# Optimization experiments

Hardware: AMD Instinct MI355X
Metric: run time of the kernel (lower is better)

## Reference

```python
import jax, jax.numpy as jnp
import numpy as np

B, S, E, H = 4, 2048, 1024, 16
DK = E // H

def setup_inputs() -> dict:
    key = jax.random.key(0)
    ks = jax.random.split(key, 5)
    scale = 1.0 / np.sqrt(E)
    return {
        "x":  jax.random.normal(ks[0], (B, S, E), dtype=jnp.float32),
        "Wq": jax.random.normal(ks[1], (E, E), dtype=jnp.float32) * scale,
        "Wk": jax.random.normal(ks[2], (E, E), dtype=jnp.float32) * scale,
        "Wv": jax.random.normal(ks[3], (E, E), dtype=jnp.float32) * scale,
        "Wo": jax.random.normal(ks[4], (E, E), dtype=jnp.float32) * scale,
    }

def reference(x, Wq, Wk, Wv, Wo):
    b, s, e = x.shape
    # nn.Linear (no bias): y = x @ W.T
    def split_heads(t):  # (b, s, e) -> (b, H, s, DK)
        return t.reshape(b, s, H, DK).transpose(0, 2, 1, 3)
    Q = split_heads(x @ Wq.T)
    K = split_heads(x @ Wk.T)
    V = split_heads(x @ Wv.T)
    scores = jnp.einsum('bhqd,bhkd->bhqk', Q, K) / jnp.sqrt(jnp.float32(DK))
    attn = jax.nn.softmax(scores, axis=-1)  # dropout p=0.0 -> identity
    ctx = jnp.einsum('bhqk,bhkd->bhqd', attn, V)
    concat = ctx.transpose(0, 2, 1, 3).reshape(b, s, e)
    return concat @ Wo.T
```

## Files before the change

### kernel.cpp

```cpp
#include <hip/hip_runtime.h>


typedef __bf16 bf16x8 __attribute__((ext_vector_type(8)));
typedef __bf16 bf16x4 __attribute__((ext_vector_type(4)));
typedef float floatx4 __attribute__((ext_vector_type(4)));

#define GLOAD_LDS16(gp, lp) __builtin_amdgcn_global_load_lds( \
    (const __attribute__((address_space(1))) unsigned int*)(gp), \
    (__attribute__((address_space(3))) unsigned int*)(lp), 16, 0, 0)

__global__ __launch_bounds__(256) void cvt_x(const float4* __restrict__ s,
                                             bf16x4* __restrict__ d, int n4) {
    int i = blockIdx.x * 256 + threadIdx.x;
    if (i < n4) {
        float4 v = s[i];
        bf16x4 o = { (__bf16)v.x, (__bf16)v.y, (__bf16)v.z, (__bf16)v.w };
        d[i] = o;
    }
}

__global__ __launch_bounds__(256) void cvt_w(const float4* __restrict__ Wq,
                                             const float4* __restrict__ Wk,
                                             const float4* __restrict__ Wv,
                                             const float4* __restrict__ Wo,
                                             bf16x4* __restrict__ oq, bf16x4* __restrict__ ok,
                                             bf16x4* __restrict__ ov, bf16x4* __restrict__ oo,
                                             float qscale) {
    int y = blockIdx.y;
    const float4* s = (y == 0) ? Wq : (y == 1) ? Wk : (y == 2) ? Wv : Wo;
    bf16x4* d = (y == 0) ? oq : (y == 1) ? ok : (y == 2) ? ov : oo;
    float scale = (y == 0) ? qscale : 1.0f;
    int i = blockIdx.x * 256 + threadIdx.x;
    float4 v = s[i];
    bf16x4 o = { (__bf16)(v.x * scale), (__bf16)(v.y * scale),
                 (__bf16)(v.z * scale), (__bf16)(v.w * scale) };
    d[i] = o;
}


__device__ __forceinline__ void gemm_mainloop(const __bf16* __restrict__ A,
                                              const __bf16* __restrict__ W,
                                              __bf16* Asm, __bf16* Bsm,
                                              int bm, int bn, int tid,
                                              floatx4 acc[4][4]) {
    const int w = tid >> 6, lane = tid & 63;
    const int quad = lane >> 4, l15 = lane & 15;
    const int wy = w >> 1, wx = w & 1;
#pragma unroll
    for (int i = 0; i < 4; ++i)
#pragma unroll
        for (int j = 0; j < 4; ++j) acc[i][j] = (floatx4){0.f, 0.f, 0.f, 0.f};

    for (int k0 = 0; k0 < 1024; k0 += 32) {
        __syncthreads();
#pragma unroll
        for (int j = 0; j < 2; ++j) {
            int base = j * 256 + w * 64;
            int flat = base + lane;
            int c = flat >> 7, r = flat & 127;
            GLOAD_LDS16(A + (size_t)(bm + r) * 1024 + k0 + c * 8, (char*)Asm + base * 16);
            GLOAD_LDS16(W + (size_t)(bn + r) * 1024 + k0 + c * 8, (char*)Bsm + base * 16);
        }
        __syncthreads();

        bf16x8 af[4], bf[4];
#pragma unroll
        for (int mt = 0; mt < 4; ++mt)
            af[mt] = *(const bf16x8*)(Asm + (quad * 128 + wy * 64 + mt * 16 + l15) * 8);
#pragma unroll
        for (int nt = 0; nt < 4; ++nt)
            bf[nt] = *(const bf16x8*)(Bsm + (quad * 128 + wx * 64 + nt * 16 + l15) * 8);
#pragma unroll
        for (int mt = 0; mt < 4; ++mt)
#pragma unroll
            for (int nt = 0; nt < 4; ++nt)
                acc[mt][nt] = __builtin_amdgcn_mfma_f32_16x16x32_bf16(af[mt], bf[nt],
                                                                      acc[mt][nt], 0, 0, 0);
    }
    __syncthreads();
}

__global__ __launch_bounds__(256) void gemm_qkv(const __bf16* __restrict__ A,
                                                const __bf16* __restrict__ Wqb,
                                                const __bf16* __restrict__ Wkb,
                                                const __bf16* __restrict__ Wvb,
                                                __bf16* __restrict__ Qg,
                                                __bf16* __restrict__ Kg,
                                                __bf16* __restrict__ Vtg) {
    __shared__ alignas(16) __bf16 Asm[4096];
    __shared__ alignas(16) __bf16 Bsm[4096];
    const int sel = blockIdx.y >> 3;
    const __bf16* W = (sel == 0) ? Wqb : (sel == 1) ? Wkb : Wvb;
    __bf16* ob = (sel == 0) ? Qg : (sel == 1) ? Kg : Vtg;
    const int bm = blockIdx.x * 128, bn = (blockIdx.y & 7) * 128;
    const int tid = threadIdx.x;
    const int w = tid >> 6, lane = tid & 63;
    const int quad = lane >> 4, l15 = lane & 15;
    const int wy = w >> 1, wx = w & 1;

    floatx4 acc[4][4];
    gemm_mainloop(A, W, Asm, Bsm, bm, bn, tid, acc);

    float* tb = (float*)Asm + w * 272;
    const int rr = lane >> 2, c0 = (lane & 3) * 4;
#pragma unroll
    for (int mt = 0; mt < 4; ++mt)
#pragma unroll
        for (int nt = 0; nt < 4; ++nt) {
            if (sel == 2) {
#pragma unroll
                for (int r = 0; r < 4; ++r) tb[l15 * 17 + quad * 4 + r] = acc[mt][nt][r];
            } else {
#pragma unroll
                for (int r = 0; r < 4; ++r) tb[(quad * 4 + r) * 17 + l15] = acc[mt][nt][r];
            }
            float f0 = tb[rr * 17 + c0 + 0], f1 = tb[rr * 17 + c0 + 1];
            float f2 = tb[rr * 17 + c0 + 2], f3 = tb[rr * 17 + c0 + 3];
            bf16x4 pk = { (__bf16)f0, (__bf16)f1, (__bf16)f2, (__bf16)f3 };
            if (sel <= 1) {
                int m = bm + wy * 64 + mt * 16 + rr;
                int n0 = bn + wx * 64 + nt * 16 + c0;
                int bI = m >> 11, s = m & 2047, h = n0 >> 6, d0 = n0 & 63;
                *(bf16x4*)(ob + ((size_t)(bI * 16 + h) * 2048 + s) * 64 + d0) = pk;
            } else {
                int m0 = bm + wy * 64 + mt * 16 + c0;
                int n = bn + wx * 64 + nt * 16 + rr;
                int bI = m0 >> 11, s0 = m0 & 2047, h = n >> 6, d = n & 63;
                *(bf16x4*)(ob + ((size_t)(bI * 16 + h) * 64 + d) * 2048 + s0) = pk;
            }
        }
}

template <int MODE>
__global__ __launch_bounds__(256) void gemm_bt(const __bf16* __restrict__ A,
                                               const __bf16* __restrict__ W,
                                               void* __restrict__ outp) {
    __shared__ alignas(16) __bf16 Asm[4096];
    __shared__ alignas(16) __bf16 Bsm[4096];
    const int tid = threadIdx.x;
    const int lane = tid & 63, w = tid >> 6;
    const int quad = lane >> 4, l15 = lane & 15;
    const int wy = w >> 1, wx = w & 1;
    const int bm = blockIdx.x * 128, bn = blockIdx.y * 128;

    floatx4 acc[4][4];
    gemm_mainloop(A, W, Asm, Bsm, bm, bn, tid, acc);

    float* of = (float*)outp;
#pragma unroll
    for (int mt = 0; mt < 4; ++mt)
#pragma unroll
        for (int nt = 0; nt < 4; ++nt)
#pragma unroll
            for (int r = 0; r < 4; ++r) {
                int m = bm + wy * 64 + mt * 16 + quad * 4 + r;
                int n = bn + wx * 64 + nt * 16 + l15;
                of[(size_t)m * 1024 + n] = acc[mt][nt][r];
            }
}


__device__ __forceinline__ int paddr(int c, int row) {
    int r2 = row ^ (((row >> 3) & 1) << 1) ^ (c & 1);
    return (c * 32 + r2) * 16;
}

__global__ __launch_bounds__(256, 4) void attn_kernel(const __bf16* __restrict__ Qg,
                                                      const __bf16* __restrict__ Kg,
                                                      const __bf16* __restrict__ Vtg,
                                                      __bf16* __restrict__ ctxg) {
    __shared__ alignas(16) __bf16 Ksm[4096];
    __shared__ alignas(16) __bf16 Vsm[4096];
    __shared__ alignas(16) __bf16 Pex[4096];
    const int tid = threadIdx.x;
    const int w = tid >> 6, lane = tid & 63;
    const int quad = lane >> 4, l15 = lane & 15;
    const int qbase = blockIdx.x * 128;
    const int bh = blockIdx.y;

    char* Pw = (w < 2) ? ((char*)Ksm + w * 4096) : ((char*)Pex + (w - 2) * 4096);

    bf16x8 qf[2][2];
#pragma unroll
    for (int mt = 0; mt < 2; ++mt) {
        const __bf16* qrow = Qg + ((size_t)bh * 2048 + qbase + w * 32 + mt * 16 + l15) * 64;
        qf[mt][0] = *(const bf16x8*)(qrow + quad * 8);
        qf[mt][1] = *(const bf16x8*)(qrow + 32 + quad * 8);
    }

    float l_p[2][4] = {{0.f, 0.f, 0.f, 0.f}, {0.f, 0.f, 0.f, 0.f}};
    floatx4 o[2][4];
#pragma unroll
    for (int mt = 0; mt < 2; ++mt)
#pragma unroll
        for (int dt = 0; dt < 4; ++dt) o[mt][dt] = (floatx4){0.f, 0.f, 0.f, 0.f};

    for (int kv = 0; kv < 32; ++kv) {
        const int kv0 = kv * 64;
        __syncthreads();
#pragma unroll
        for (int j = 0; j < 2; ++j) {
            int base = j * 256 + w * 64;
            int flat = base + lane;
            int c = flat >> 6, r = flat & 63;
            GLOAD_LDS16(Kg + ((size_t)bh * 2048 + kv0 + r) * 64 + c * 8, (char*)Ksm + base * 16);
            GLOAD_LDS16(Vtg + ((size_t)bh * 64 + r) * 2048 + kv0 + c * 8, (char*)Vsm + base * 16);
        }
        __syncthreads();

        floatx4 sa[2][4];
#pragma unroll
        for (int mt = 0; mt < 2; ++mt)
#pragma unroll
            for (int nt = 0; nt < 4; ++nt) sa[mt][nt] = (floatx4){0.f, 0.f, 0.f, 0.f};
#pragma unroll
        for (int nt = 0; nt < 4; ++nt) {
            bf16x8 kb0 = *(const bf16x8*)(Ksm + (quad * 64 + nt * 16 + l15) * 8);
            bf16x8 kb1 = *(const bf16x8*)(Ksm + ((4 + quad) * 64 + nt * 16 + l15) * 8);
#pragma unroll
            for (int mt = 0; mt < 2; ++mt) {
                sa[mt][nt] = __builtin_amdgcn_mfma_f32_16x16x32_bf16(qf[mt][0], kb0,
                                                                    sa[mt][nt], 0, 0, 0);
                sa[mt][nt] = __builtin_amdgcn_mfma_f32_16x16x32_bf16(qf[mt][1], kb1,
                                                                    sa[mt][nt], 0, 0, 0);
            }
        }

        __syncthreads();

#pragma unroll
        for (int mt = 0; mt < 2; ++mt)
#pragma unroll
            for (int nt = 0; nt < 4; ++nt)
#pragma unroll
                for (int r = 0; r < 4; ++r) {
                    float p = __builtin_amdgcn_exp2f(sa[mt][nt][r]);
                    l_p[mt][r] += p;
                    unsigned u = __builtin_bit_cast(unsigned, p);
                    *(unsigned short*)(Pw + paddr(nt * 2 + (l15 >> 3),
                                                  mt * 16 + quad * 4 + r)
                                       + (l15 & 7) * 2) = (unsigned short)(u >> 16);
                }

#pragma unroll
        for (int kk = 0; kk < 2; ++kk) {
            bf16x8 pa0 = *(const bf16x8*)(Pw + paddr(kk * 4 + quad, l15));
            bf16x8 pa1 = *(const bf16x8*)(Pw + paddr(kk * 4 + quad, 16 + l15));
#pragma unroll
            for (int dt = 0; dt < 4; ++dt) {
                bf16x8 vb = *(const bf16x8*)(Vsm + ((kk * 4 + quad) * 64 + dt * 16 + l15) * 8);
                o[0][dt] = __builtin_amdgcn_mfma_f32_16x16x32_bf16(pa0, vb, o[0][dt], 0, 0, 0);
                o[1][dt] = __builtin_amdgcn_mfma_f32_16x16x32_bf16(pa1, vb, o[1][dt], 0, 0, 0);
            }
        }
    }

    __syncthreads();

    float inv[2][4];
#pragma unroll
    for (int mt = 0; mt < 2; ++mt)
#pragma unroll
        for (int r = 0; r < 4; ++r) {
            float t = l_p[mt][r];
            t += __shfl_xor(t, 1); t += __shfl_xor(t, 2);
            t += __shfl_xor(t, 4); t += __shfl_xor(t, 8);
            inv[mt][r] = 1.f / t;
        }

    float* tb = (float*)Ksm + w * 272;
    const int bI = bh >> 4, h = bh & 15;
    const int rr = lane >> 2, c0 = (lane & 3) * 4;
#pragma unroll
    for (int mt = 0; mt < 2; ++mt)
#pragma unroll
        for (int dt = 0; dt < 4; ++dt) {
#pragma unroll
            for (int r = 0; r < 4; ++r)
                tb[(quad * 4 + r) * 17 + l15] = o[mt][dt][r] * inv[mt][r];
            float f0 = tb[rr * 17 + c0 + 0], f1 = tb[rr * 17 + c0 + 1];
            float f2 = tb[rr * 17 + c0 + 2], f3 = tb[rr * 17 + c0 + 3];
            bf16x4 pk = { (__bf16)f0, (__bf16)f1, (__bf16)f2, (__bf16)f3 };
            *(bf16x4*)(ctxg + ((size_t)(bI * 2048 + qbase + w * 32 + mt * 16 + rr)) * 1024
                       + h * 64 + dt * 16 + c0) = pk;
        }
}

extern "C" void kernel_launch(void* const* d_in, const int* in_sizes, int n_in,
                              void* d_out, int out_size, void* d_ws, size_t ws_size,
                              hipStream_t stream) {
    const float* x  = (const float*)d_in[0];
    const float* Wq = (const float*)d_in[1];
    const float* Wk = (const float*)d_in[2];
    const float* Wv = (const float*)d_in[3];
    const float* Wo = (const float*)d_in[4];
    float* out = (float*)d_out;
    char* ws = (char*)d_ws;

    __bf16* xb  = (__bf16*)(ws);
    __bf16* wqb = (__bf16*)(ws + (16u << 20));
    __bf16* wkb = (__bf16*)(ws + (18u << 20));
    __bf16* wvb = (__bf16*)(ws + (20u << 20));
    __bf16* wob = (__bf16*)(ws + (22u << 20));
    __bf16* Qg  = (__bf16*)(ws + (24u << 20));
    __bf16* Kg  = (__bf16*)(ws + (40u << 20));
    __bf16* Vtg = (__bf16*)(ws + (56u << 20));
    __bf16* ctx = xb;

    const float qscale = 0.18033688011112042f;

    cvt_x<<<8192, 256, 0, stream>>>((const float4*)x, (bf16x4*)xb, 2097152);
    cvt_w<<<dim3(1024, 4), 256, 0, stream>>>((const float4*)Wq, (const float4*)Wk,
                                             (const float4*)Wv, (const float4*)Wo,
                                             (bf16x4*)wqb, (bf16x4*)wkb,
                                             (bf16x4*)wvb, (bf16x4*)wob, qscale);

    gemm_qkv<<<dim3(64, 24), 256, 0, stream>>>(xb, wqb, wkb, wvb, Qg, Kg, Vtg);

    attn_kernel<<<dim3(16, 64), 256, 0, stream>>>(Qg, Kg, Vtg, ctx);

    gemm_bt<3><<<dim3(64, 8), 256, 0, stream>>>(ctx, wob, (void*)out);
}
```

Measured before the change: 337.6 us.

## Double-buffer GEMM LDS tiles and give attention its own P buffer

The shared GEMM mainloop now keeps two LDS stages and issues the global-to-LDS loads for tile k+1 before computing on tile k, with one barrier per iteration instead of two. The aim is to overlap global memory latency with MFMA work in the QKV and output projections, and the launch bounds now ask for 5 blocks per SM. The attention kernel gets a dedicated P scratch buffer instead of reusing the K tile for two waves, which lets it drop one __syncthreads per KV step. The cost is twice the LDS per GEMM block and more LDS in attention, which may lower occupancy.

```diff
diff --git a/kernel.cpp b/kernel.cpp
--- a/kernel.cpp
+++ b/kernel.cpp
@@ -38,9 +38,26 @@
 }
 
 
+__device__ __forceinline__ void gemm_stage(const __bf16* __restrict__ A,
+                                           const __bf16* __restrict__ W,
+                                           __bf16* SM, int buf,
+                                           int bm, int bn, int k0,
+                                           int w, int lane) {
+#pragma unroll
+    for (int j = 0; j < 2; ++j) {
+        int base = j * 256 + w * 64;
+        int flat = base + lane;
+        int c = flat >> 7, r = flat & 127;
+        GLOAD_LDS16(A + (size_t)(bm + r) * 1024 + k0 + c * 8,
+                    (char*)(SM + buf * 8192) + base * 16);
+        GLOAD_LDS16(W + (size_t)(bn + r) * 1024 + k0 + c * 8,
+                    (char*)(SM + buf * 8192 + 4096) + base * 16);
+    }
+}
+
 __device__ __forceinline__ void gemm_mainloop(const __bf16* __restrict__ A,
                                               const __bf16* __restrict__ W,
-                                              __bf16* Asm, __bf16* Bsm,
+                                              __bf16* SM,
                                               int bm, int bn, int tid,
                                               floatx4 acc[4][4]) {
     const int w = tid >> 6, lane = tid & 63;
@@ -51,18 +68,14 @@
 #pragma unroll
         for (int j = 0; j < 4; ++j) acc[i][j] = (floatx4){0.f, 0.f, 0.f, 0.f};
 
-    for (int k0 = 0; k0 < 1024; k0 += 32) {
-        __syncthreads();
-#pragma unroll
-        for (int j = 0; j < 2; ++j) {
-            int base = j * 256 + w * 64;
-            int flat = base + lane;
-            int c = flat >> 7, r = flat & 127;
-            GLOAD_LDS16(A + (size_t)(bm + r) * 1024 + k0 + c * 8, (char*)Asm + base * 16);
-            GLOAD_LDS16(W + (size_t)(bn + r) * 1024 + k0 + c * 8, (char*)Bsm + base * 16);
-        }
-        __syncthreads();
-
+    gemm_stage(A, W, SM, 0, bm, bn, 0, w, lane);
+    __syncthreads();
+
+    for (int k = 0; k < 32; ++k) {
+        if (k + 1 < 32) gemm_stage(A, W, SM, (k + 1) & 1, bm, bn, (k + 1) * 32, w, lane);
+
+        const __bf16* Asm = SM + (k & 1) * 8192;
+        const __bf16* Bsm = Asm + 4096;
         bf16x8 af[4], bf[4];
 #pragma unroll
         for (int mt = 0; mt < 4; ++mt)
@@ -76,19 +89,18 @@
             for (int nt = 0; nt < 4; ++nt)
                 acc[mt][nt] = __builtin_amdgcn_mfma_f32_16x16x32_bf16(af[mt], bf[nt],
                                                                       acc[mt][nt], 0, 0, 0);
-    }
-    __syncthreads();
-}
-
-__global__ __launch_bounds__(256) void gemm_qkv(const __bf16* __restrict__ A,
-                                                const __bf16* __restrict__ Wqb,
-                                                const __bf16* __restrict__ Wkb,
-                                                const __bf16* __restrict__ Wvb,
-                                                __bf16* __restrict__ Qg,
-                                                __bf16* __restrict__ Kg,
-                                                __bf16* __restrict__ Vtg) {
-    __shared__ alignas(16) __bf16 Asm[4096];
-    __shared__ alignas(16) __bf16 Bsm[4096];
+        __syncthreads();
+    }
+}
+
+__global__ __launch_bounds__(256, 5) void gemm_qkv(const __bf16* __restrict__ A,
+                                                   const __bf16* __restrict__ Wqb,
+                                                   const __bf16* __restrict__ Wkb,
+                                                   const __bf16* __restrict__ Wvb,
+                                                   __bf16* __restrict__ Qg,
+                                                   __bf16* __restrict__ Kg,
+                                                   __bf16* __restrict__ Vtg) {
+    __shared__ alignas(16) __bf16 SM[16384];
     const int sel = blockIdx.y >> 3;
     const __bf16* W = (sel == 0) ? Wqb : (sel == 1) ? Wkb : Wvb;
     __bf16* ob = (sel == 0) ? Qg : (sel == 1) ? Kg : Vtg;
@@ -99,9 +111,9 @@
     const int wy = w >> 1, wx = w & 1;
 
     floatx4 acc[4][4];
-    gemm_mainloop(A, W, Asm, Bsm, bm, bn, tid, acc);
-
-    float* tb = (float*)Asm + w * 272;
+    gemm_mainloop(A, W, SM, bm, bn, tid, acc);
+
+    float* tb = (float*)SM + w * 272;
     const int rr = lane >> 2, c0 = (lane & 3) * 4;
 #pragma unroll
     for (int mt = 0; mt < 4; ++mt)
@@ -132,11 +144,10 @@
 }
 
 template <int MODE>
-__global__ __launch_bounds__(256) void gemm_bt(const __bf16* __restrict__ A,
-                                               const __bf16* __restrict__ W,
-                                               void* __restrict__ outp) {
-    __shared__ alignas(16) __bf16 Asm[4096];
-    __shared__ alignas(16) __bf16 Bsm[4096];
+__global__ __launch_bounds__(256, 5) void gemm_bt(const __bf16* __restrict__ A,
+                                                  const __bf16* __restrict__ W,
+                                                  void* __restrict__ outp) {
+    __shared__ alignas(16) __bf16 SM[16384];
     const int tid = threadIdx.x;
     const int lane = tid & 63, w = tid >> 6;
     const int quad = lane >> 4, l15 = lane & 15;
@@ -144,7 +155,7 @@
     const int bm = blockIdx.x * 128, bn = blockIdx.y * 128;
 
     floatx4 acc[4][4];
-    gemm_mainloop(A, W, Asm, Bsm, bm, bn, tid, acc);
+    gemm_mainloop(A, W, SM, bm, bn, tid, acc);
 
     float* of = (float*)outp;
 #pragma unroll
@@ -171,14 +182,14 @@
                                                       __bf16* __restrict__ ctxg) {
     __shared__ alignas(16) __bf16 Ksm[4096];
     __shared__ alignas(16) __bf16 Vsm[4096];
-    __shared__ alignas(16) __bf16 Pex[4096];
+    __shared__ alignas(16) __bf16 Psm[8192];
     const int tid = threadIdx.x;
     const int w = tid >> 6, lane = tid & 63;
     const int quad = lane >> 4, l15 = lane & 15;
     const int qbase = blockIdx.x * 128;
     const int bh = blockIdx.y;
 
-    char* Pw = (w < 2) ? ((char*)Ksm + w * 4096) : ((char*)Pex + (w - 2) * 4096);
+    char* Pw = (char*)Psm + w * 4096;
 
     bf16x8 qf[2][2];
 #pragma unroll
@@ -225,8 +236,6 @@
                                                                     sa[mt][nt], 0, 0, 0);
             }
         }
-
-        __syncthreads();
 
 #pragma unroll
         for (int mt = 0; mt < 2; ++mt)
```

Result: slower. 347.0 us (+2.8%).

## Widen GEMM tiles to 128x256 and give attention a dedicated P buffer

Applied to the files above, without the earlier changes.

Both projection GEMMs now use 128x256 block tiles: each wave computes 64x128 with 4x8 MFMA accumulators, and the grid is reordered so N-blocks vary fastest. This is meant to raise arithmetic intensity per LDS load and improve reuse of the A rows. The attention kernel gets its own 16KB P scratch buffer instead of aliasing the K shared memory, which removes one __syncthreads per KV iteration. The cost is more shared memory and registers per block (launch bounds of 2 for the GEMMs), so occupancy drops. Fewer GEMM blocks also risks filling the CUs less evenly.

```diff
diff --git a/kernel.cpp b/kernel.cpp
--- a/kernel.cpp
+++ b/kernel.cpp
@@ -38,18 +38,20 @@
 }
 
 
-__device__ __forceinline__ void gemm_mainloop(const __bf16* __restrict__ A,
-                                              const __bf16* __restrict__ W,
-                                              __bf16* Asm, __bf16* Bsm,
-                                              int bm, int bn, int tid,
-                                              floatx4 acc[4][4]) {
+__device__ __forceinline__ void gemm_mainloop2(const __bf16* __restrict__ A,
+                                               const __bf16* __restrict__ W,
+                                               __bf16* SM,
+                                               int bm, int bn, int tid,
+                                               floatx4 acc[4][8]) {
     const int w = tid >> 6, lane = tid & 63;
     const int quad = lane >> 4, l15 = lane & 15;
     const int wy = w >> 1, wx = w & 1;
+    __bf16* Asm = SM;
+    __bf16* Bsm = SM + 4096;
 #pragma unroll
     for (int i = 0; i < 4; ++i)
 #pragma unroll
-        for (int j = 0; j < 4; ++j) acc[i][j] = (floatx4){0.f, 0.f, 0.f, 0.f};
+        for (int j = 0; j < 8; ++j) acc[i][j] = (floatx4){0.f, 0.f, 0.f, 0.f};
 
     for (int k0 = 0; k0 < 1024; k0 += 32) {
         __syncthreads();
@@ -59,54 +61,59 @@
             int flat = base + lane;
             int c = flat >> 7, r = flat & 127;
             GLOAD_LDS16(A + (size_t)(bm + r) * 1024 + k0 + c * 8, (char*)Asm + base * 16);
+        }
+#pragma unroll
+        for (int j = 0; j < 4; ++j) {
+            int base = j * 256 + w * 64;
+            int flat = base + lane;
+            int c = flat >> 8, r = flat & 255;
             GLOAD_LDS16(W + (size_t)(bn + r) * 1024 + k0 + c * 8, (char*)Bsm + base * 16);
         }
         __syncthreads();
 
-        bf16x8 af[4], bf[4];
+        bf16x8 af[4], bf[8];
 #pragma unroll
         for (int mt = 0; mt < 4; ++mt)
             af[mt] = *(const bf16x8*)(Asm + (quad * 128 + wy * 64 + mt * 16 + l15) * 8);
 #pragma unroll
-        for (int nt = 0; nt < 4; ++nt)
-            bf[nt] = *(const bf16x8*)(Bsm + (quad * 128 + wx * 64 + nt * 16 + l15) * 8);
+        for (int nt = 0; nt < 8; ++nt)
+            bf[nt] = *(const bf16x8*)(Bsm + (quad * 256 + wx * 128 + nt * 16 + l15) * 8);
 #pragma unroll
         for (int mt = 0; mt < 4; ++mt)
 #pragma unroll
-            for (int nt = 0; nt < 4; ++nt)
+            for (int nt = 0; nt < 8; ++nt)
                 acc[mt][nt] = __builtin_amdgcn_mfma_f32_16x16x32_bf16(af[mt], bf[nt],
                                                                       acc[mt][nt], 0, 0, 0);
     }
     __syncthreads();
 }
 
-__global__ __launch_bounds__(256) void gemm_qkv(const __bf16* __restrict__ A,
-                                                const __bf16* __restrict__ Wqb,
-                                                const __bf16* __restrict__ Wkb,
-                                                const __bf16* __restrict__ Wvb,
-                                                __bf16* __restrict__ Qg,
-                                                __bf16* __restrict__ Kg,
-                                                __bf16* __restrict__ Vtg) {
-    __shared__ alignas(16) __bf16 Asm[4096];
-    __shared__ alignas(16) __bf16 Bsm[4096];
-    const int sel = blockIdx.y >> 3;
+__global__ __launch_bounds__(256, 2) void gemm_qkv(const __bf16* __restrict__ A,
+                                                   const __bf16* __restrict__ Wqb,
+                                                   const __bf16* __restrict__ Wkb,
+                                                   const __bf16* __restrict__ Wvb,
+                                                   __bf16* __restrict__ Qg,
+                                                   __bf16* __restrict__ Kg,
+                                                   __bf16* __restrict__ Vtg) {
+    __shared__ alignas(16) __bf16 SM[12288];
+    const int sel = blockIdx.x >> 2;
     const __bf16* W = (sel == 0) ? Wqb : (sel == 1) ? Wkb : Wvb;
     __bf16* ob = (sel == 0) ? Qg : (sel == 1) ? Kg : Vtg;
-    const int bm = blockIdx.x * 128, bn = (blockIdx.y & 7) * 128;
+    const int bm = blockIdx.y * 128, bn = (blockIdx.x & 3) * 256;
     const int tid = threadIdx.x;
     const int w = tid >> 6, lane = tid & 63;
     const int quad = lane >> 4, l15 = lane & 15;
     const int wy = w >> 1, wx = w & 1;
 
-    floatx4 acc[4][4];
-    gemm_mainloop(A, W, Asm, Bsm, bm, bn, tid, acc);
-
-    float* tb = (float*)Asm + w * 272;
+    floatx4 acc[4][8];
+    gemm_mainloop2(A, W, SM, bm, bn, tid, acc);
+
+    float* tb = (float*)SM + w * 272;
     const int rr = lane >> 2, c0 = (lane & 3) * 4;
 #pragma unroll
     for (int mt = 0; mt < 4; ++mt)
 #pragma unroll
-        for (int nt = 0; nt < 4; ++nt) {
+        for (int nt = 0; nt < 8; ++nt) {
             if (sel == 2) {
 #pragma unroll
                 for (int r = 0; r < 4; ++r) tb[l15 * 17 + quad * 4 + r] = acc[mt][nt][r];
@@ -119,42 +126,39 @@
             bf16x4 pk = { (__bf16)f0, (__bf16)f1, (__bf16)f2, (__bf16)f3 };
             if (sel <= 1) {
                 int m = bm + wy * 64 + mt * 16 + rr;
-                int n0 = bn + wx * 64 + nt * 16 + c0;
+                int n0 = bn + wx * 128 + nt * 16 + c0;
                 int bI = m >> 11, s = m & 2047, h = n0 >> 6, d0 = n0 & 63;
                 *(bf16x4*)(ob + ((size_t)(bI * 16 + h) * 2048 + s) * 64 + d0) = pk;
             } else {
                 int m0 = bm + wy * 64 + mt * 16 + c0;
-                int n = bn + wx * 64 + nt * 16 + rr;
+                int n = bn + wx * 128 + nt * 16 + rr;
                 int bI = m0 >> 11, s0 = m0 & 2047, h = n >> 6, d = n & 63;
                 *(bf16x4*)(ob + ((size_t)(bI * 16 + h) * 64 + d) * 2048 + s0) = pk;
             }
         }
 }
 
-template <int MODE>
-__global__ __launch_bounds__(256) void gemm_bt(const __bf16* __restrict__ A,
-                                               const __bf16* __restrict__ W,
-                                               void* __restrict__ outp) {
-    __shared__ alignas(16) __bf16 Asm[4096];
-    __shared__ alignas(16) __bf16 Bsm[4096];
+__global__ __launch_bounds__(256, 2) void gemm_out(const __bf16* __restrict__ A,
+                                                   const __bf16* __restrict__ W,
+                                                   float* __restrict__ of) {
+    __shared__ alignas(16) __bf16 SM[12288];
     const int tid = threadIdx.x;
     const int lane = tid & 63, w = tid >> 6;
     const int quad = lane >> 4, l15 = lane & 15;
     const int wy = w >> 1, wx = w & 1;
-    const int bm = blockIdx.x * 128, bn = blockIdx.y * 128;
-
-    floatx4 acc[4][4];
-    gemm_mainloop(A, W, Asm, Bsm, bm, bn, tid, acc);
-
-    float* of = (float*)outp;
+    const int bm = blockIdx.y * 128, bn = blockIdx.x * 256;
+
+    floatx4 acc[4][8];
+    gemm_mainloop2(A, W, SM, bm, bn, tid, acc);
+
 #pragma unroll
     for (int mt = 0; mt < 4; ++mt)
 #pragma unroll
-        for (int nt = 0; nt < 4; ++nt)
+        for (int nt = 0; nt < 8; ++nt)
 #pragma unroll
             for (int r = 0; r < 4; ++r) {
                 int m = bm + wy * 64 + mt * 16 + quad * 4 + r;
-                int n = bn + wx * 64 + nt * 16 + l15;
+                int n = bn + wx * 128 + nt * 16 + l15;
                 of[(size_t)m * 1024 + n] = acc[mt][nt][r];
             }
 }
@@ -171,14 +175,14 @@
                                                       __bf16* __restrict__ ctxg) {
     __shared__ alignas(16) __bf16 Ksm[4096];
     __shared__ alignas(16) __bf16 Vsm[4096];
-    __shared__ alignas(16) __bf16 Pex[4096];
+    __shared__ alignas(16) __bf16 Psm[8192];
     const int tid = threadIdx.x;
     const int w = tid >> 6, lane = tid & 63;
     const int quad = lane >> 4, l15 = lane & 15;
     const int qbase = blockIdx.x * 128;
     const int bh = blockIdx.y;
 
-    char* Pw = (w < 2) ? ((char*)Ksm + w * 4096) : ((char*)Pex + (w - 2) * 4096);
+    char* Pw = (char*)Psm + w * 4096;
 
     bf16x8 qf[2][2];
 #pragma unroll
@@ -225,8 +229,6 @@
                                                                     sa[mt][nt], 0, 0, 0);
             }
         }
-
-        __syncthreads();
 
 #pragma unroll
         for (int mt = 0; mt < 2; ++mt)
@@ -315,9 +317,9 @@
                                              (bf16x4*)wqb, (bf16x4*)wkb,
                                              (bf16x4*)wvb, (bf16x4*)wob, qscale);
 
-    gemm_qkv<<<dim3(64, 24), 256, 0, stream>>>(xb, wqb, wkb, wvb, Qg, Kg, Vtg);
+    gemm_qkv<<<dim3(12, 64), 256, 0, stream>>>(xb, wqb, wkb, wvb, Qg, Kg, Vtg);
 
     attn_kernel<<<dim3(16, 64), 256, 0, stream>>>(Qg, Kg, Vtg, ctx);
 
-    gemm_bt<3><<<dim3(64, 8), 256, 0, stream>>>(ctx, wob, (void*)out);
-}
+    gemm_out<<<dim3(4, 64), 256, 0, stream>>>(ctx, wob, out);
+}
```

After: 336.4 us. Within noise of the previous version (-0.4%).
